# Optimization experiments

Measured on AMD Instinct MI355X. Metric: run time of the kernel, lower is better.

The kernel has to match this reference:

```python
import jax, jax.numpy as jnp
import numpy as np

B, L, A, D, H = 4, 1024, 8, 1024, 16
DK = D // H


def setup_inputs() -> dict:
    key = jax.random.key(0)
    ks = jax.random.split(key, 11)
    s = 1.0 / np.sqrt(D)
    return {
        "query": jax.random.normal(ks[0], (B, L, A, D), jnp.float32),
        "key": jax.random.normal(ks[1], (B, L, A, D), jnp.float32),
        "value": jax.random.normal(ks[2], (B, L, A, D), jnp.float32),
        "Wq": jax.random.uniform(ks[3], (D, D), jnp.float32, -s, s),
        "bq": jax.random.uniform(ks[4], (D,), jnp.float32, -s, s),
        "Wk": jax.random.uniform(ks[5], (D, D), jnp.float32, -s, s),
        "bk": jax.random.uniform(ks[6], (D,), jnp.float32, -s, s),
        "Wv": jax.random.uniform(ks[7], (D, D), jnp.float32, -s, s),
        "bv": jax.random.uniform(ks[8], (D,), jnp.float32, -s, s),
        "Wo": jax.random.uniform(ks[9], (D, D), jnp.float32, -s, s),
        "bo": jax.random.uniform(ks[10], (D,), jnp.float32, -s, s),
        "d_atrbt": A,
    }


def _proj_heads(x, W, b, a):
    # torch nn.Linear: x @ W.T + b; then view [B, L, a, H, DK] and transpose(2,3)
    y = jnp.einsum("blad,ed->blae", x, W) + b
    nb, nl = y.shape[0], y.shape[1]
    return y.reshape(nb, nl, a, H, DK).transpose(0, 1, 3, 2, 4)  # [B, L, H, a, DK]


def reference(query, key, value, Wq, bq, Wk, bk, Wv, bv, Wo, bo, d_atrbt):
    a = d_atrbt
    q = _proj_heads(query, Wq, bq, a)
    k = _proj_heads(key, Wk, bk, a)
    v = _proj_heads(value, Wv, bv, a)
    # scaled dot-product attention over the attribute axis (size a) per token
    scores = jnp.einsum("blhad,blhed->blhae", q, k) / jnp.sqrt(jnp.asarray(DK, q.dtype))
    p = jax.nn.softmax(scores, axis=-1)  # [B, L, H, a, a]
    x = jnp.einsum("blhae,blhed->blhad", p, v)  # [B, L, H, a, DK]
    nb, nl = x.shape[0], x.shape[1]
    x = x.transpose(0, 1, 3, 2, 4).reshape(nb, nl, a, H * DK)  # [B, L, a, D]
    return jnp.einsum("blad,ed->blae", x, Wo) + bo
```

## Files before the change

kernel.cpp:

```cpp
#include <hip/hip_runtime.h>
#include <hip/hip_bf16.h>
#include <stdint.h>

typedef unsigned short u16;
typedef __bf16 bf16x8 __attribute__((ext_vector_type(8)));
typedef float f32x4 __attribute__((ext_vector_type(4)));

#define MROWS 32768
#define NDIM  1024
#define KDIM  1024
#define NKT   16

__device__ __forceinline__ void gload_lds16(const void* g, void* l) {
  __builtin_amdgcn_global_load_lds(
      (__attribute__((address_space(1))) const void*)g,
      (__attribute__((address_space(3))) void*)l,
      16, 0, 0);
}

struct CvtArgs { const float* s[4]; u16* d[4]; };
struct ProjArgs {
  const float* A[3]; const u16* W[3]; const float* bias[3]; u16* C[3];
};

__global__ __launch_bounds__(256) void cvt4_kernel(CvtArgs ca) {
  const int which = blockIdx.x >> 9;
  const float* s = ca.s[which];
  u16* d = ca.d[which];
  const int i = ((((int)blockIdx.x & 511) * 256) + (int)threadIdx.x) * 8;
  const float4 f0 = *(const float4*)(s + i);
  const float4 f1 = *(const float4*)(s + i + 4);
  bf16x8 h;
  h[0] = (__bf16)f0.x; h[1] = (__bf16)f0.y; h[2] = (__bf16)f0.z; h[3] = (__bf16)f0.w;
  h[4] = (__bf16)f1.x; h[5] = (__bf16)f1.y; h[6] = (__bf16)f1.z; h[7] = (__bf16)f1.w;
  *(bf16x8*)((void*)(d + i)) = h;
}


#define GEMM_COMMON_IDX()                                                     \
  const int t = (int)threadIdx.x;                                             \
  const int lane = t & 63;                                                    \
  const int wid = t >> 6;                                                     \
  const int wm = wid >> 2;                                                    \
  const int wn = wid & 3;                                                     \
  const int fr = lane & 15;                                                   \
  const int hi = lane >> 4;

__global__ __launch_bounds__(512, 2) void proj3_kernel(ProjArgs pa) {
  __shared__ __align__(16) unsigned char As[2][32768];
  __shared__ __align__(16) unsigned char Bs[2][32768];

  const int bid = (int)blockIdx.x;
  const int xcd = bid & 7;
  const int within = bid >> 3;
  const int g = within >> 6;
  const int w2 = within & 63;
  const int by = xcd * 16 + (w2 >> 2);
  const int bx = w2 & 3;

  const float* Af = pa.A[g];
  const u16* Bw = pa.W[g];
  const float* bias = pa.bias[g];
  u16* C = pa.C[g];

  GEMM_COMMON_IDX();

  size_t bG[4]; int bL[4];
#pragma unroll
  for (int i = 0; i < 4; ++i) {
    const int idx = i * 512 + t;
    const int r = idx >> 3, ch = idx & 7;
    bG[i] = (size_t)(bx * 256 + r) * KDIM + (size_t)((ch ^ (r & 7)) << 3);
    bL[i] = (i * 512 + (t & ~63)) * 16;
  }

  const int ra = t >> 1;
  const float* gA = Af + (size_t)(by * 256 + ra) * KDIM + (t & 1) * 32;
  int wA[4];
#pragma unroll
  for (int c = 0; c < 4; ++c)
    wA[c] = ra * 128 + (((((t & 1) * 4) + c) ^ (ra & 7)) << 4);

  int aRow[8], bRow[4], colx[2];
#pragma unroll
  for (int m = 0; m < 8; ++m) aRow[m] = (wm * 128 + m * 16 + fr) * 128;
#pragma unroll
  for (int n = 0; n < 4; ++n) bRow[n] = (wn * 64 + n * 16 + fr) * 128;
#pragma unroll
  for (int kk = 0; kk < 2; ++kk) colx[kk] = (((kk * 4 + hi) ^ (fr & 7)) << 4);

  f32x4 acc[8][4] = {};
  float4 pf[8];

#pragma unroll
  for (int i = 0; i < 8; ++i) pf[i] = ((const float4*)gA)[i];
#pragma unroll
  for (int i = 0; i < 4; ++i) gload_lds16(Bw + bG[i], &Bs[0][bL[i]]);

  for (int kt = 0; kt < NKT; ++kt) {
    const int cur = kt & 1, nxt = cur ^ 1;

#pragma unroll
    for (int c = 0; c < 4; ++c) {
      bf16x8 h;
      h[0] = (__bf16)pf[2 * c].x; h[1] = (__bf16)pf[2 * c].y;
      h[2] = (__bf16)pf[2 * c].z; h[3] = (__bf16)pf[2 * c].w;
      h[4] = (__bf16)pf[2 * c + 1].x; h[5] = (__bf16)pf[2 * c + 1].y;
      h[6] = (__bf16)pf[2 * c + 1].z; h[7] = (__bf16)pf[2 * c + 1].w;
      *(bf16x8*)((void*)&As[cur][wA[c]]) = h;
    }
    __syncthreads();

    bf16x8 bf0[4], a0[4];
#pragma unroll
    for (int n = 0; n < 4; ++n)
      bf0[n] = *(const bf16x8*)((const void*)&Bs[cur][bRow[n] + colx[0]]);
#pragma unroll
    for (int m = 0; m < 4; ++m)
      a0[m] = *(const bf16x8*)((const void*)&As[cur][aRow[m] + colx[0]]);

    if (kt + 1 < NKT) {
      const int ko = (kt + 1) * 64;
      const float* g2 = gA + ko;
#pragma unroll
      for (int i = 0; i < 8; ++i) pf[i] = ((const float4*)g2)[i];
#pragma unroll
      for (int i = 0; i < 4; ++i)
        gload_lds16(Bw + bG[i] + ko, &Bs[nxt][bL[i]]);
    }

    __builtin_amdgcn_s_setprio(1);
#pragma unroll
    for (int m = 0; m < 4; ++m)
#pragma unroll
      for (int n = 0; n < 4; ++n)
        acc[m][n] = __builtin_amdgcn_mfma_f32_16x16x32_bf16(a0[m], bf0[n], acc[m][n], 0, 0, 0);
    __builtin_amdgcn_s_setprio(0);

#pragma unroll
    for (int m = 0; m < 4; ++m)
      a0[m] = *(const bf16x8*)((const void*)&As[cur][aRow[4 + m] + colx[0]]);
    __builtin_amdgcn_s_setprio(1);
#pragma unroll
    for (int m = 0; m < 4; ++m)
#pragma unroll
      for (int n = 0; n < 4; ++n)
        acc[4 + m][n] = __builtin_amdgcn_mfma_f32_16x16x32_bf16(a0[m], bf0[n], acc[4 + m][n], 0, 0, 0);
    __builtin_amdgcn_s_setprio(0);

#pragma unroll
    for (int n = 0; n < 4; ++n)
      bf0[n] = *(const bf16x8*)((const void*)&Bs[cur][bRow[n] + colx[1]]);
#pragma unroll
    for (int m = 0; m < 4; ++m)
      a0[m] = *(const bf16x8*)((const void*)&As[cur][aRow[m] + colx[1]]);
    __builtin_amdgcn_s_setprio(1);
#pragma unroll
    for (int m = 0; m < 4; ++m)
#pragma unroll
      for (int n = 0; n < 4; ++n)
        acc[m][n] = __builtin_amdgcn_mfma_f32_16x16x32_bf16(a0[m], bf0[n], acc[m][n], 0, 0, 0);
    __builtin_amdgcn_s_setprio(0);
#pragma unroll
    for (int m = 0; m < 4; ++m)
      a0[m] = *(const bf16x8*)((const void*)&As[cur][aRow[4 + m] + colx[1]]);
    __builtin_amdgcn_s_setprio(1);
#pragma unroll
    for (int m = 0; m < 4; ++m)
#pragma unroll
      for (int n = 0; n < 4; ++n)
        acc[4 + m][n] = __builtin_amdgcn_mfma_f32_16x16x32_bf16(a0[m], bf0[n], acc[4 + m][n], 0, 0, 0);
    __builtin_amdgcn_s_setprio(0);
  }

  const int row0 = by * 256 + wm * 128 + hi * 4;
  const int col0 = bx * 256 + wn * 64 + fr;
#pragma unroll
  for (int n = 0; n < 4; ++n) {
    const int gc = col0 + n * 16;
    const float bv = bias[gc];
#pragma unroll
    for (int m = 0; m < 8; ++m) {
#pragma unroll
      for (int j = 0; j < 4; ++j) {
        const size_t idx = (size_t)(row0 + m * 16 + j) * NDIM + (size_t)gc;
        C[idx] = __builtin_bit_cast(u16, (__bf16)(acc[m][n][j] + bv));
      }
    }
  }
}

__global__ __launch_bounds__(512, 2) void gemmo_kernel(const u16* __restrict__ Ab,
                                                       const u16* __restrict__ Bw,
                                                       const float* __restrict__ bias,
                                                       float* __restrict__ C) {
  __shared__ __align__(16) unsigned char As[2][32768];
  __shared__ __align__(16) unsigned char Bs[2][32768];

  const int bid = (int)blockIdx.x;
  const int xcd = bid & 7;
  const int within = bid >> 3;
  const int by = xcd * 16 + (within >> 2);
  const int bx = within & 3;

  GEMM_COMMON_IDX();

  size_t aG[4], bG[4]; int aL[4], bL[4];
#pragma unroll
  for (int i = 0; i < 4; ++i) {
    const int idx = i * 512 + t;
    const int r = idx >> 3, ch = idx & 7;
    const size_t cswz = (size_t)((ch ^ (r & 7)) << 3);
    aG[i] = (size_t)(by * 256 + r) * KDIM + cswz;
    bG[i] = (size_t)(bx * 256 + r) * KDIM + cswz;
    aL[i] = bL[i] = (i * 512 + (t & ~63)) * 16;
  }

  int aRow[8], bRow[4], colx[2];
#pragma unroll
  for (int m = 0; m < 8; ++m) aRow[m] = (wm * 128 + m * 16 + fr) * 128;
#pragma unroll
  for (int n = 0; n < 4; ++n) bRow[n] = (wn * 64 + n * 16 + fr) * 128;
#pragma unroll
  for (int kk = 0; kk < 2; ++kk) colx[kk] = (((kk * 4 + hi) ^ (fr & 7)) << 4);

  f32x4 acc[8][4] = {};

#pragma unroll
  for (int i = 0; i < 4; ++i) {
    gload_lds16(Ab + aG[i], &As[0][aL[i]]);
    gload_lds16(Bw + bG[i], &Bs[0][bL[i]]);
  }

  for (int kt = 0; kt < NKT; ++kt) {
    const int cur = kt & 1, nxt = cur ^ 1;
    __syncthreads();

    bf16x8 bf0[4], a0[4];
#pragma unroll
    for (int n = 0; n < 4; ++n)
      bf0[n] = *(const bf16x8*)((const void*)&Bs[cur][bRow[n] + colx[0]]);
#pragma unroll
    for (int m = 0; m < 4; ++m)
      a0[m] = *(const bf16x8*)((const void*)&As[cur][aRow[m] + colx[0]]);

    if (kt + 1 < NKT) {
      const int ko = (kt + 1) * 64;
#pragma unroll
      for (int i = 0; i < 4; ++i) {
        gload_lds16(Ab + aG[i] + ko, &As[nxt][aL[i]]);
        gload_lds16(Bw + bG[i] + ko, &Bs[nxt][bL[i]]);
      }
    }

    __builtin_amdgcn_s_setprio(1);
#pragma unroll
    for (int m = 0; m < 4; ++m)
#pragma unroll
      for (int n = 0; n < 4; ++n)
        acc[m][n] = __builtin_amdgcn_mfma_f32_16x16x32_bf16(a0[m], bf0[n], acc[m][n], 0, 0, 0);
    __builtin_amdgcn_s_setprio(0);
#pragma unroll
    for (int m = 0; m < 4; ++m)
      a0[m] = *(const bf16x8*)((const void*)&As[cur][aRow[4 + m] + colx[0]]);
    __builtin_amdgcn_s_setprio(1);
#pragma unroll
    for (int m = 0; m < 4; ++m)
#pragma unroll
      for (int n = 0; n < 4; ++n)
        acc[4 + m][n] = __builtin_amdgcn_mfma_f32_16x16x32_bf16(a0[m], bf0[n], acc[4 + m][n], 0, 0, 0);
    __builtin_amdgcn_s_setprio(0);

#pragma unroll
    for (int n = 0; n < 4; ++n)
      bf0[n] = *(const bf16x8*)((const void*)&Bs[cur][bRow[n] + colx[1]]);
#pragma unroll
    for (int m = 0; m < 4; ++m)
      a0[m] = *(const bf16x8*)((const void*)&As[cur][aRow[m] + colx[1]]);
    __builtin_amdgcn_s_setprio(1);
#pragma unroll
    for (int m = 0; m < 4; ++m)
#pragma unroll
      for (int n = 0; n < 4; ++n)
        acc[m][n] = __builtin_amdgcn_mfma_f32_16x16x32_bf16(a0[m], bf0[n], acc[m][n], 0, 0, 0);
    __builtin_amdgcn_s_setprio(0);
#pragma unroll
    for (int m = 0; m < 4; ++m)
      a0[m] = *(const bf16x8*)((const void*)&As[cur][aRow[4 + m] + colx[1]]);
    __builtin_amdgcn_s_setprio(1);
#pragma unroll
    for (int m = 0; m < 4; ++m)
#pragma unroll
      for (int n = 0; n < 4; ++n)
        acc[4 + m][n] = __builtin_amdgcn_mfma_f32_16x16x32_bf16(a0[m], bf0[n], acc[4 + m][n], 0, 0, 0);
    __builtin_amdgcn_s_setprio(0);
  }

  const int row0 = by * 256 + wm * 128 + hi * 4;
  const int col0 = bx * 256 + wn * 64 + fr;
#pragma unroll
  for (int n = 0; n < 4; ++n) {
    const int gc = col0 + n * 16;
    const float bv = bias[gc];
#pragma unroll
    for (int m = 0; m < 8; ++m) {
#pragma unroll
      for (int j = 0; j < 4; ++j) {
        const size_t idx = (size_t)(row0 + m * 16 + j) * NDIM + (size_t)gc;
        C[idx] = acc[m][n][j] + bv;
      }
    }
  }
}

__global__ __launch_bounds__(256) void attn_kernel(u16* __restrict__ qx,
                                                   const u16* __restrict__ kb,
                                                   const u16* __restrict__ vb) {
  __shared__ __align__(16) u16 qs[4][8][64];
  __shared__ __align__(16) u16 ks[4][8][64];
  __shared__ __align__(16) u16 vs[4][8][64];
  const int t = threadIdx.x;
  const int lane = t & 63;
  const int w = t >> 6;
  const int unit = blockIdx.x * 4 + w;
  const int bl = unit >> 4;
  const int h = unit & 15;
  const int row = lane >> 3;
  const int c8 = (lane & 7) * 8;
  const size_t goff = (size_t)bl * 8 * 1024 + (size_t)h * 64 + (size_t)row * 1024 + c8;

  *(int4*)((void*)&qs[w][row][c8]) = *(const int4*)((const void*)&qx[goff]);
  *(int4*)((void*)&ks[w][row][c8]) = *(const int4*)((const void*)&kb[goff]);
  *(int4*)((void*)&vs[w][row][c8]) = *(const int4*)((const void*)&vb[goff]);
  __syncthreads();

  const int a = row;
  const int e = lane & 7;
  float s = 0.f;
#pragma unroll
  for (int d8 = 0; d8 < 64; d8 += 8) {
    const bf16x8 qv = *(const bf16x8*)((const void*)&qs[w][a][d8]);
    const bf16x8 kv = *(const bf16x8*)((const void*)&ks[w][e][d8]);
#pragma unroll
    for (int j = 0; j < 8; ++j) s += (float)qv[j] * (float)kv[j];
  }
  s *= 0.125f;

  float mx = s;
#pragma unroll
  for (int o = 1; o < 8; o <<= 1) mx = fmaxf(mx, __shfl_xor(mx, o));
  float p = __expf(s - mx);
  float sum = p;
#pragma unroll
  for (int o = 1; o < 8; o <<= 1) sum += __shfl_xor(sum, o);
  p /= sum;

  float xo[8] = {};
#pragma unroll
  for (int e2 = 0; e2 < 8; ++e2) {
    const float pe = __shfl(p, (lane & 56) + e2);
    const bf16x8 vv = *(const bf16x8*)((const void*)&vs[w][e2][c8]);
#pragma unroll
    for (int j = 0; j < 8; ++j) xo[j] += pe * (float)vv[j];
  }
  bf16x8 hx;
#pragma unroll
  for (int j = 0; j < 8; ++j) hx[j] = (__bf16)xo[j];
  *(int4*)((void*)&qx[goff]) = __builtin_bit_cast(int4, hx);
}

extern "C" void kernel_launch(void* const* d_in, const int* in_sizes, int n_in,
                              void* d_out, int out_size, void* d_ws, size_t ws_size,
                              hipStream_t stream) {
  const float* query = (const float*)d_in[0];
  const float* key   = (const float*)d_in[1];
  const float* value = (const float*)d_in[2];
  const float* Wq = (const float*)d_in[3];
  const float* bq = (const float*)d_in[4];
  const float* Wk = (const float*)d_in[5];
  const float* bk = (const float*)d_in[6];
  const float* Wv = (const float*)d_in[7];
  const float* bv = (const float*)d_in[8];
  const float* Wo = (const float*)d_in[9];
  const float* bo = (const float*)d_in[10];
  (void)in_sizes; (void)n_in; (void)out_size; (void)ws_size;

  const size_t mn = (size_t)MROWS * (size_t)NDIM;

  u16* kb = (u16*)d_out;
  u16* vb = kb + mn;
  u16* qb = (u16*)d_ws;
  u16* Wqb = qb + mn;
  u16* Wkb = Wqb + 1048576;
  u16* Wvb = Wkb + 1048576;
  u16* Wob = Wvb + 1048576;

  CvtArgs ca;
  ca.s[0] = Wq; ca.s[1] = Wk; ca.s[2] = Wv; ca.s[3] = Wo;
  ca.d[0] = Wqb; ca.d[1] = Wkb; ca.d[2] = Wvb; ca.d[3] = Wob;
  cvt4_kernel<<<2048, 256, 0, stream>>>(ca);

  ProjArgs pa;
  pa.A[0] = key;  pa.A[1] = value; pa.A[2] = query;
  pa.W[0] = Wkb;  pa.W[1] = Wvb;   pa.W[2] = Wqb;
  pa.bias[0] = bk; pa.bias[1] = bv; pa.bias[2] = bq;
  pa.C[0] = kb;   pa.C[1] = vb;    pa.C[2] = qb;
  proj3_kernel<<<1536, 512, 0, stream>>>(pa);

  attn_kernel<<<16384, 256, 0, stream>>>(qb, kb, vb);

  gemmo_kernel<<<512, 512, 0, stream>>>(qb, Wob, bo, (float*)d_out);
}
```

Measured before the change: 544.1 us.

## Split projections into half-batch fp32-to-bf16 conversion plus bf16 GEMM passes

Replaces the fused projection kernel, which read fp32 activations and converted them to bf16 inside the GEMM loop, with a separate conversion pass. Each half of each input (Q, K, V) is converted into a bf16 scratch buffer, then a shared templated bf16 GEMM that loads both operands directly into LDS consumes it. The goal is to cut fp32 register traffic and in-loop conversion work in the GEMM. In exchange it adds an extra global write and read of the activations, six extra kernel launches, and smaller GEMM grids of 256 blocks each.

```diff
diff --git a/kernel.cpp b/kernel.cpp
--- a/kernel.cpp
+++ b/kernel.cpp
@@ -10,6 +10,7 @@
 #define NDIM  1024
 #define KDIM  1024
 #define NKT   16
+#define MHALF 16777216
 
 __device__ __forceinline__ void gload_lds16(const void* g, void* l) {
   __builtin_amdgcn_global_load_lds(
@@ -19,9 +20,6 @@
 }
 
 struct CvtArgs { const float* s[4]; u16* d[4]; };
-struct ProjArgs {
-  const float* A[3]; const u16* W[3]; const float* bias[3]; u16* C[3];
-};
 
 __global__ __launch_bounds__(256) void cvt4_kernel(CvtArgs ca) {
   const int which = blockIdx.x >> 9;
@@ -36,174 +34,39 @@
   *(bf16x8*)((void*)(d + i)) = h;
 }
 
-
-#define GEMM_COMMON_IDX()                                                     \
-  const int t = (int)threadIdx.x;                                             \
-  const int lane = t & 63;                                                    \
-  const int wid = t >> 6;                                                     \
-  const int wm = wid >> 2;                                                    \
-  const int wn = wid & 3;                                                     \
-  const int fr = lane & 15;                                                   \
-  const int hi = lane >> 4;
-
-__global__ __launch_bounds__(512, 2) void proj3_kernel(ProjArgs pa) {
+__global__ __launch_bounds__(256) void cvt_half_kernel(const float* __restrict__ s,
+                                                       u16* __restrict__ d) {
+  const int i = ((int)blockIdx.x * 256 + (int)threadIdx.x) * 8;
+  const float4 f0 = *(const float4*)(s + i);
+  const float4 f1 = *(const float4*)(s + i + 4);
+  bf16x8 h;
+  h[0] = (__bf16)f0.x; h[1] = (__bf16)f0.y; h[2] = (__bf16)f0.z; h[3] = (__bf16)f0.w;
+  h[4] = (__bf16)f1.x; h[5] = (__bf16)f1.y; h[6] = (__bf16)f1.z; h[7] = (__bf16)f1.w;
+  *(bf16x8*)((void*)(d + i)) = h;
+}
+
+template <bool OUT_F32>
+__global__ __launch_bounds__(512, 2) void gemm_bt256(const u16* __restrict__ Ab,
+                                                     const u16* __restrict__ Bw,
+                                                     const float* __restrict__ bias,
+                                                     void* __restrict__ Cv,
+                                                     int byPerXcd) {
   __shared__ __align__(16) unsigned char As[2][32768];
   __shared__ __align__(16) unsigned char Bs[2][32768];
 
   const int bid = (int)blockIdx.x;
   const int xcd = bid & 7;
   const int within = bid >> 3;
-  const int g = within >> 6;
-  const int w2 = within & 63;
-  const int by = xcd * 16 + (w2 >> 2);
-  const int bx = w2 & 3;
-
-  const float* Af = pa.A[g];
-  const u16* Bw = pa.W[g];
-  const float* bias = pa.bias[g];
-  u16* C = pa.C[g];
-
-  GEMM_COMMON_IDX();
-
-  size_t bG[4]; int bL[4];
-#pragma unroll
-  for (int i = 0; i < 4; ++i) {
-    const int idx = i * 512 + t;
-    const int r = idx >> 3, ch = idx & 7;
-    bG[i] = (size_t)(bx * 256 + r) * KDIM + (size_t)((ch ^ (r & 7)) << 3);
-    bL[i] = (i * 512 + (t & ~63)) * 16;
-  }
-
-  const int ra = t >> 1;
-  const float* gA = Af + (size_t)(by * 256 + ra) * KDIM + (t & 1) * 32;
-  int wA[4];
-#pragma unroll
-  for (int c = 0; c < 4; ++c)
-    wA[c] = ra * 128 + (((((t & 1) * 4) + c) ^ (ra & 7)) << 4);
-
-  int aRow[8], bRow[4], colx[2];
-#pragma unroll
-  for (int m = 0; m < 8; ++m) aRow[m] = (wm * 128 + m * 16 + fr) * 128;
-#pragma unroll
-  for (int n = 0; n < 4; ++n) bRow[n] = (wn * 64 + n * 16 + fr) * 128;
-#pragma unroll
-  for (int kk = 0; kk < 2; ++kk) colx[kk] = (((kk * 4 + hi) ^ (fr & 7)) << 4);
-
-  f32x4 acc[8][4] = {};
-  float4 pf[8];
-
-#pragma unroll
-  for (int i = 0; i < 8; ++i) pf[i] = ((const float4*)gA)[i];
-#pragma unroll
-  for (int i = 0; i < 4; ++i) gload_lds16(Bw + bG[i], &Bs[0][bL[i]]);
-
-  for (int kt = 0; kt < NKT; ++kt) {
-    const int cur = kt & 1, nxt = cur ^ 1;
-
-#pragma unroll
-    for (int c = 0; c < 4; ++c) {
-      bf16x8 h;
-      h[0] = (__bf16)pf[2 * c].x; h[1] = (__bf16)pf[2 * c].y;
-      h[2] = (__bf16)pf[2 * c].z; h[3] = (__bf16)pf[2 * c].w;
-      h[4] = (__bf16)pf[2 * c + 1].x; h[5] = (__bf16)pf[2 * c + 1].y;
-      h[6] = (__bf16)pf[2 * c + 1].z; h[7] = (__bf16)pf[2 * c + 1].w;
-      *(bf16x8*)((void*)&As[cur][wA[c]]) = h;
-    }
-    __syncthreads();
-
-    bf16x8 bf0[4], a0[4];
-#pragma unroll
-    for (int n = 0; n < 4; ++n)
-      bf0[n] = *(const bf16x8*)((const void*)&Bs[cur][bRow[n] + colx[0]]);
-#pragma unroll
-    for (int m = 0; m < 4; ++m)
-      a0[m] = *(const bf16x8*)((const void*)&As[cur][aRow[m] + colx[0]]);
-
-    if (kt + 1 < NKT) {
-      const int ko = (kt + 1) * 64;
-      const float* g2 = gA + ko;
-#pragma unroll
-      for (int i = 0; i < 8; ++i) pf[i] = ((const float4*)g2)[i];
-#pragma unroll
-      for (int i = 0; i < 4; ++i)
-        gload_lds16(Bw + bG[i] + ko, &Bs[nxt][bL[i]]);
-    }
-
-    __builtin_amdgcn_s_setprio(1);
-#pragma unroll
-    for (int m = 0; m < 4; ++m)
-#pragma unroll
-      for (int n = 0; n < 4; ++n)
-        acc[m][n] = __builtin_amdgcn_mfma_f32_16x16x32_bf16(a0[m], bf0[n], acc[m][n], 0, 0, 0);
-    __builtin_amdgcn_s_setprio(0);
-
-#pragma unroll
-    for (int m = 0; m < 4; ++m)
-      a0[m] = *(const bf16x8*)((const void*)&As[cur][aRow[4 + m] + colx[0]]);
-    __builtin_amdgcn_s_setprio(1);
-#pragma unroll
-    for (int m = 0; m < 4; ++m)
-#pragma unroll
-      for (int n = 0; n < 4; ++n)
-        acc[4 + m][n] = __builtin_amdgcn_mfma_f32_16x16x32_bf16(a0[m], bf0[n], acc[4 + m][n], 0, 0, 0);
-    __builtin_amdgcn_s_setprio(0);
-
-#pragma unroll
-    for (int n = 0; n < 4; ++n)
-      bf0[n] = *(const bf16x8*)((const void*)&Bs[cur][bRow[n] + colx[1]]);
-#pragma unroll
-    for (int m = 0; m < 4; ++m)
-      a0[m] = *(const bf16x8*)((const void*)&As[cur][aRow[m] + colx[1]]);
-    __builtin_amdgcn_s_setprio(1);
-#pragma unroll
-    for (int m = 0; m < 4; ++m)
-#pragma unroll
-      for (int n = 0; n < 4; ++n)
-        acc[m][n] = __builtin_amdgcn_mfma_f32_16x16x32_bf16(a0[m], bf0[n], acc[m][n], 0, 0, 0);
-    __builtin_amdgcn_s_setprio(0);
-#pragma unroll
-    for (int m = 0; m < 4; ++m)
-      a0[m] = *(const bf16x8*)((const void*)&As[cur][aRow[4 + m] + colx[1]]);
-    __builtin_amdgcn_s_setprio(1);
-#pragma unroll
-    for (int m = 0; m < 4; ++m)
-#pragma unroll
-      for (int n = 0; n < 4; ++n)
-        acc[4 + m][n] = __builtin_amdgcn_mfma_f32_16x16x32_bf16(a0[m], bf0[n], acc[4 + m][n], 0, 0, 0);
-    __builtin_amdgcn_s_setprio(0);
-  }
-
-  const int row0 = by * 256 + wm * 128 + hi * 4;
-  const int col0 = bx * 256 + wn * 64 + fr;
-#pragma unroll
-  for (int n = 0; n < 4; ++n) {
-    const int gc = col0 + n * 16;
-    const float bv = bias[gc];
-#pragma unroll
-    for (int m = 0; m < 8; ++m) {
-#pragma unroll
-      for (int j = 0; j < 4; ++j) {
-        const size_t idx = (size_t)(row0 + m * 16 + j) * NDIM + (size_t)gc;
-        C[idx] = __builtin_bit_cast(u16, (__bf16)(acc[m][n][j] + bv));
-      }
-    }
-  }
-}
-
-__global__ __launch_bounds__(512, 2) void gemmo_kernel(const u16* __restrict__ Ab,
-                                                       const u16* __restrict__ Bw,
-                                                       const float* __restrict__ bias,
-                                                       float* __restrict__ C) {
-  __shared__ __align__(16) unsigned char As[2][32768];
-  __shared__ __align__(16) unsigned char Bs[2][32768];
-
-  const int bid = (int)blockIdx.x;
-  const int xcd = bid & 7;
-  const int within = bid >> 3;
-  const int by = xcd * 16 + (within >> 2);
+  const int by = xcd * byPerXcd + (within >> 2);
   const int bx = within & 3;
 
-  GEMM_COMMON_IDX();
+  const int t = (int)threadIdx.x;
+  const int lane = t & 63;
+  const int wid = t >> 6;
+  const int wm = wid >> 2;
+  const int wn = wid & 3;
+  const int fr = lane & 15;
+  const int hi = lane >> 4;
 
   size_t aG[4], bG[4]; int aL[4], bL[4];
 #pragma unroll
@@ -307,7 +170,11 @@
 #pragma unroll
       for (int j = 0; j < 4; ++j) {
         const size_t idx = (size_t)(row0 + m * 16 + j) * NDIM + (size_t)gc;
-        C[idx] = acc[m][n][j] + bv;
+        const float val = acc[m][n][j] + bv;
+        if constexpr (OUT_F32)
+          ((float*)Cv)[idx] = val;
+        else
+          ((u16*)Cv)[idx] = __builtin_bit_cast(u16, (__bf16)val);
       }
     }
   }
@@ -394,20 +261,26 @@
   u16* Wkb = Wqb + 1048576;
   u16* Wvb = Wkb + 1048576;
   u16* Wob = Wvb + 1048576;
+  u16* Abf = Wob + 1048576;
 
   CvtArgs ca;
   ca.s[0] = Wq; ca.s[1] = Wk; ca.s[2] = Wv; ca.s[3] = Wo;
   ca.d[0] = Wqb; ca.d[1] = Wkb; ca.d[2] = Wvb; ca.d[3] = Wob;
   cvt4_kernel<<<2048, 256, 0, stream>>>(ca);
 
-  ProjArgs pa;
-  pa.A[0] = key;  pa.A[1] = value; pa.A[2] = query;
-  pa.W[0] = Wkb;  pa.W[1] = Wvb;   pa.W[2] = Wqb;
-  pa.bias[0] = bk; pa.bias[1] = bv; pa.bias[2] = bq;
-  pa.C[0] = kb;   pa.C[1] = vb;    pa.C[2] = qb;
-  proj3_kernel<<<1536, 512, 0, stream>>>(pa);
+  const float* srcs[3] = {key, value, query};
+  const u16* wts[3] = {Wkb, Wvb, Wqb};
+  const float* bss[3] = {bk, bv, bq};
+  u16* outs[3] = {kb, vb, qb};
+  for (int g = 0; g < 3; ++g) {
+    for (int h = 0; h < 2; ++h) {
+      cvt_half_kernel<<<8192, 256, 0, stream>>>(srcs[g] + (size_t)h * MHALF, Abf);
+      gemm_bt256<false><<<256, 512, 0, stream>>>(
+          Abf, wts[g], bss[g], (void*)(outs[g] + (size_t)h * MHALF), 8);
+    }
+  }
 
   attn_kernel<<<16384, 256, 0, stream>>>(qb, kb, vb);
 
-  gemmo_kernel<<<512, 512, 0, stream>>>(qb, Wob, bo, (float*)d_out);
-}
+  gemm_bt256<true><<<512, 512, 0, stream>>>(qb, Wob, bo, d_out, 16);
+}
```

Measured after the change: 494.9 us. 1.1x faster.
